# Optimization experiments

Hardware: AMD Instinct MI355X
Metric: run time of the kernel (lower is better)

## Reference

```python
import jax, jax.numpy as jnp
import numpy as np

B, S, DIM = 1, 2048, 2048
NH, NKV, HD = 32, 8, 64
NREP = NH // NKV  # 4


def setup_inputs() -> dict:
    key = jax.random.key(0)
    ks = jax.random.split(key, 5)
    x = jax.random.normal(ks[0], (B, S, DIM), jnp.float32)
    # torch nn.Linear weight layout: (out_features, in_features)
    wq = jax.random.normal(ks[1], (NH * HD, DIM), jnp.float32) * (DIM ** -0.5)
    wk = jax.random.normal(ks[2], (NKV * HD, DIM), jnp.float32) * (DIM ** -0.5)
    wv = jax.random.normal(ks[3], (NKV * HD, DIM), jnp.float32) * (DIM ** -0.5)
    wo = jax.random.normal(ks[4], (DIM, NH * HD), jnp.float32) * ((NH * HD) ** -0.5)
    # Llama-style rotary frequencies: angle[t, i] = t / 10000^(2i/head_dim)
    inv_freq = 1.0 / (10000.0 ** (np.arange(0, HD, 2, dtype=np.float64) / HD))  # (HD/2,)
    ang = np.outer(np.arange(S, dtype=np.float64), inv_freq)                     # (S, HD/2)
    freqs_cis = jnp.asarray(np.stack([np.cos(ang), np.sin(ang)], axis=-1), jnp.float32)  # (S, HD/2, 2)
    # additive causal mask, shape (1, 1, S, S)
    mask = jnp.triu(jnp.full((S, S), -1e9, jnp.float32), k=1)[None, None]
    return dict(x=x, wq=wq, wk=wk, wv=wv, wo=wo, freqs_cis=freqs_cis, mask=mask)


def _apply_rope(x, cos, sin):
    # x: (B, S, H, HD); rotate adjacent pairs along last dim
    xr = x.reshape(x.shape[:-1] + (-1, 2))
    x1, x2 = xr[..., 0], xr[..., 1]
    c = cos[None, :, None, :]  # (1, S, 1, HD/2)
    s = sin[None, :, None, :]
    out = jnp.stack([x1 * c - x2 * s, x1 * s + x2 * c], axis=-1)
    return out.reshape(x.shape)


def reference(x, wq, wk, wv, wo, freqs_cis, mask):
    b, s, _ = x.shape
    q = (x @ wq.T).reshape(b, s, NH, HD)
    k = (x @ wk.T).reshape(b, s, NKV, HD)
    v = (x @ wv.T).reshape(b, s, NKV, HD)
    cos, sin = freqs_cis[..., 0], freqs_cis[..., 1]
    q = _apply_rope(q, cos, sin)
    k = _apply_rope(k, cos, sin)
    # GQA: group q heads by kv head instead of materializing repeated K/V
    qg = q.reshape(b, s, NKV, NREP, HD)
    scale = HD ** -0.5
    # scores: (b, g=kv_head, r=rep, s=q_pos, t=k_pos)
    scores = jnp.einsum('bsgrd,btgd->bgrst', qg, k) * scale
    scores = scores + mask[:, :, None]  # (1,1,1,S,S) broadcast
    p = jax.nn.softmax(scores.astype(jnp.float32), axis=-1).astype(q.dtype)
    out = jnp.einsum('bgrst,btgd->bsgrd', p, v).reshape(b, s, NH * HD)
    return out @ wo.T
```

## Files before the change

### kernel.cpp

```cpp
#include <hip/hip_runtime.h>
#include <hip/hip_bf16.h>

#define S_LEN 2048
#define DIM_  2048
#define NH    32
#define NKV   8
#define HD    64

typedef __bf16 bf16x8 __attribute__((ext_vector_type(8)));
typedef __bf16 bf16x4 __attribute__((ext_vector_type(4)));
typedef float  f32x4  __attribute__((ext_vector_type(4)));

#define AS_GLOBAL(p) ((const __attribute__((address_space(1))) void*)(p))
#define AS_LDS(p)    ((__attribute__((address_space(3))) void*)(p))

__device__ __forceinline__ bf16x8 pack8(float4 a, float4 b) {
  bf16x8 r;
  r[0] = (__bf16)a.x; r[1] = (__bf16)a.y; r[2] = (__bf16)a.z; r[3] = (__bf16)a.w;
  r[4] = (__bf16)b.x; r[5] = (__bf16)b.y; r[6] = (__bf16)b.z; r[7] = (__bf16)b.w;
  return r;
}

__global__ __launch_bounds__(256) void cvt_xw(
    const float* __restrict__ x,  const float* __restrict__ wq,
    const float* __restrict__ wk, const float* __restrict__ wv,
    const float* __restrict__ wo,
    __bf16* __restrict__ xb, __bf16* __restrict__ wb, __bf16* __restrict__ wob)
{
  const size_t stride = 458752;
  size_t base = (size_t)blockIdx.x * 256 + threadIdx.x;
#pragma unroll
  for (int k = 0; k < 4; ++k) {
    size_t i = base + (size_t)k * stride;
    const float* src; __bf16* dst; size_t j;
    if (i < 524288)       { src = x;  dst = xb;            j = i; }
    else if (i < 1048576) { src = wq; dst = wb;            j = i - 524288; }
    else if (i < 1179648) { src = wk; dst = wb + 4194304;  j = i - 1048576; }
    else if (i < 1310720) { src = wv; dst = wb + 5242880;  j = i - 1179648; }
    else                  { src = wo; dst = wob;           j = i - 1310720; }
    float4 f0 = ((const float4*)src)[j * 2];
    float4 f1 = ((const float4*)src)[j * 2 + 1];
    ((bf16x8*)dst)[j ^ ((j >> 8) & 7)] = pack8(f0, f1);
  }
}

#define BK 64
#define TA_ELEMS 8192
#define TB_ELEMS 4096

__device__ __forceinline__ void stage_A(
    const __bf16* __restrict__ g, int row0, int k0, int ld, __bf16* lds)
{
  const int tid = threadIdx.x;
  const int wave = tid >> 6;
#pragma unroll
  for (int iss = 0; iss < 4; ++iss) {
    int off = (iss * 256 + tid) * 16;
    int r = off >> 7;
    int c = (off & 127) >> 1;
    __builtin_amdgcn_global_load_lds(
        AS_GLOBAL(g + (size_t)(row0 + r) * ld + k0 + c),
        AS_LDS(lds + iss * 2048 + wave * 512),
        16, 0, 0);
  }
}

__device__ __forceinline__ void stage_B(
    const __bf16* __restrict__ g, int row0, int k0, int ld, __bf16* lds)
{
  const int tid = threadIdx.x;
  const int wave = tid >> 6;
#pragma unroll
  for (int iss = 0; iss < 2; ++iss) {
    int off = (iss * 256 + tid) * 16;
    int r = off >> 7;
    int c = (off & 127) >> 1;
    __builtin_amdgcn_global_load_lds(
        AS_GLOBAL(g + (size_t)(row0 + r) * ld + k0 + c),
        AS_LDS(lds + iss * 2048 + wave * 512), 16, 0, 0);
  }
}

__device__ __forceinline__ void gemm_mainloop(
    const __bf16* __restrict__ A, const __bf16* __restrict__ B,
    int row0, int col0, int lda, int ldb, int nt,
    __bf16* As, __bf16* Bs, f32x4 acc[4][2])
{
  const int lane = threadIdx.x & 63;
  const int wave = threadIdx.x >> 6;
  const int wr = wave >> 1, wc = wave & 1;
  const int fr = lane & 15, fg = lane >> 4;
  const int sw = fr & 7;

  stage_A(A, row0, 0, lda, As);
  stage_B(B, col0, 0, ldb, Bs);

  for (int t = 0; t < nt; ++t) {
    const int cur = t & 1;
    if (t + 1 < nt) {
      stage_A(A, row0, (t + 1) * BK, lda, As + (cur ^ 1) * TA_ELEMS);
      stage_B(B, col0, (t + 1) * BK, ldb, Bs + (cur ^ 1) * TB_ELEMS);
    }
    __syncthreads();
#pragma unroll
    for (int kk = 0; kk < 2; ++kk) {
      bf16x8 a[4], b[2];
#pragma unroll
      for (int mi = 0; mi < 4; ++mi)
        a[mi] = *(const bf16x8*)(As + cur * TA_ELEMS +
                 (wr * 64 + mi * 16 + fr) * 64 + (((kk * 4 + fg) ^ sw) * 8));
#pragma unroll
      for (int ni = 0; ni < 2; ++ni)
        b[ni] = *(const bf16x8*)(Bs + cur * TB_ELEMS +
                 (wc * 32 + ni * 16 + fr) * 64 + (((kk * 4 + fg) ^ sw) * 8));
#pragma unroll
      for (int mi = 0; mi < 4; ++mi)
#pragma unroll
        for (int ni = 0; ni < 2; ++ni)
          acc[mi][ni] = __builtin_amdgcn_mfma_f32_16x16x32_bf16(a[mi], b[ni], acc[mi][ni], 0, 0, 0);
    }
    __syncthreads();
  }
}

__global__ __launch_bounds__(256) void qkv_gemm(
    const __bf16* __restrict__ xb, const __bf16* __restrict__ wb,
    __bf16* __restrict__ q_buf, __bf16* __restrict__ k_buf, __bf16* __restrict__ v_buf)
{
  __shared__ __bf16 As[2 * TA_ELEMS];
  __shared__ __bf16 Bs[2 * TB_ELEMS];
  const int lane = threadIdx.x & 63;
  const int wave = threadIdx.x >> 6;
  const int wr = wave >> 1, wc = wave & 1;
  const int fr = lane & 15, fg = lane >> 4;

  const int lid = blockIdx.x;
  const int xcd = lid & 7;
  const int i   = lid >> 3;
  const int row0 = (i & 15) * 128;
  const int col0 = (xcd * 6 + (i >> 4)) * 64;

  f32x4 acc[4][2] = {};
  gemm_mainloop(xb, wb, row0, col0, DIM_, DIM_, DIM_ / BK, As, Bs, acc);

  const int rowg0 = row0 + wr * 64;
  const int colg0 = col0 + wc * 32;
#pragma unroll
  for (int mi = 0; mi < 4; ++mi) {
#pragma unroll
    for (int ni = 0; ni < 2; ++ni) {
#pragma unroll
      for (int j = 0; j < 4; ++j) {
        int row = rowg0 + mi * 16 + fg * 4 + j;
        int col = colg0 + ni * 16 + fr;
        float v = acc[mi][ni][j];
        if (col < 2048) {
          int h = col >> 6, d = col & 63;
          q_buf[((size_t)h * S_LEN + row) * HD + d] = (__bf16)v;
        } else if (col < 2560) {
          int c = col - 2048, g = c >> 6, d = c & 63;
          k_buf[((size_t)g * S_LEN + row) * HD + d] = (__bf16)v;
        } else {
          int c = col - 2560, g = c >> 6, d = c & 63;
          v_buf[((size_t)g * HD + d) * S_LEN + row] = (__bf16)v;
        }
      }
    }
  }
}

__global__ __launch_bounds__(256) void oproj_gemm(
    const __bf16* __restrict__ attn_buf, const __bf16* __restrict__ wob,
    float* __restrict__ out)
{
  __shared__ __bf16 As[2 * TA_ELEMS];
  __shared__ __bf16 Bs[2 * TB_ELEMS];
  const int lane = threadIdx.x & 63;
  const int wave = threadIdx.x >> 6;
  const int wr = wave >> 1, wc = wave & 1;
  const int fr = lane & 15, fg = lane >> 4;

  const int lid = blockIdx.x;
  const int xcd = lid & 7;
  const int i   = lid >> 3;
  const int row0 = (i & 15) * 128;
  const int col0 = (xcd * 4 + (i >> 4)) * 64;

  f32x4 acc[4][2] = {};
  gemm_mainloop(attn_buf, wob, row0, col0, DIM_, DIM_, DIM_ / BK, As, Bs, acc);

  const int rowg0 = row0 + wr * 64;
  const int colg0 = col0 + wc * 32;
#pragma unroll
  for (int mi = 0; mi < 4; ++mi)
#pragma unroll
    for (int ni = 0; ni < 2; ++ni)
#pragma unroll
      for (int j = 0; j < 4; ++j) {
        int row = rowg0 + mi * 16 + fg * 4 + j;
        int col = colg0 + ni * 16 + fr;
        out[(size_t)row * DIM_ + col] = acc[mi][ni][j];
      }
}

__global__ __launch_bounds__(256) void rope_k(
    __bf16* __restrict__ k_buf, const float* __restrict__ fc)
{
  int idx = blockIdx.x * 256 + threadIdx.x;
  int i    = idx & 31;
  int sp   = (idx >> 5) & (S_LEN - 1);
  int g    = idx >> 16;
  __bf16* buf = k_buf + ((size_t)g * S_LEN + sp) * HD;
  float c = fc[(sp * 32 + i) * 2 + 0];
  float s = fc[(sp * 32 + i) * 2 + 1];
  float x1 = (float)buf[2 * i], x2 = (float)buf[2 * i + 1];
  buf[2 * i + 0] = (__bf16)(x1 * c - x2 * s);
  buf[2 * i + 1] = (__bf16)(x1 * s + x2 * c);
}

__global__ __launch_bounds__(512) void attn_kernel(
    const __bf16* __restrict__ q_buf, const __bf16* __restrict__ k_buf,
    const __bf16* __restrict__ v_buf, const float* __restrict__ fc,
    __bf16* __restrict__ attn_buf)
{
  __shared__ __align__(16) __bf16 Ks[2][64 * 64];
  __shared__ __align__(16) __bf16 Vs[2][64 * 64];
  __shared__ __align__(16) __bf16 lds_p[8][16][72];

  const int tid  = threadIdx.x;
  const int lane = tid & 63;
  const int wave = tid >> 6;
  const int n = blockIdx.x;
  const int qt = (n < 256) ? (15 - (n >> 5)) : ((n - 256) >> 5);
  const int h  = n & 31;
  const int g = h >> 2;
  const int r0 = qt * 128 + wave * 16;
  const int lrow = lane & 15;
  const int lgrp = lane >> 4;
  const int lk = lgrp * 8;

  const __bf16* qh = q_buf + (size_t)h * S_LEN * HD;
  const __bf16* kh = k_buf + (size_t)g * S_LEN * HD;
  const __bf16* vh = v_buf + (size_t)g * HD * S_LEN;

  const int sr   = tid >> 3;
  const int scol = tid & 7;
  const int dcol = scol ^ (sr & 7);

  const float KS = 0.125f * 1.44269504088896f;
  bf16x8 qa[2];
  const float* fcrow = fc + (size_t)(r0 + lrow) * 64;
#pragma unroll
  for (int kk = 0; kk < 2; ++kk) {
    qa[kk] = *(const bf16x8*)(qh + (size_t)(r0 + lrow) * HD + kk * 32 + lk);
    float4 cs0 = *(const float4*)(fcrow + (kk * 16 + lgrp * 4) * 2);
    float4 cs1 = *(const float4*)(fcrow + (kk * 16 + lgrp * 4) * 2 + 4);
    float cc[4] = {cs0.x * KS, cs0.z * KS, cs1.x * KS, cs1.z * KS};
    float ss[4] = {cs0.y * KS, cs0.w * KS, cs1.y * KS, cs1.w * KS};
#pragma unroll
    for (int pr = 0; pr < 4; ++pr) {
      float x1 = (float)qa[kk][2 * pr], x2 = (float)qa[kk][2 * pr + 1];
      qa[kk][2 * pr]     = (__bf16)(x1 * cc[pr] - x2 * ss[pr]);
      qa[kk][2 * pr + 1] = (__bf16)(x1 * ss[pr] + x2 * cc[pr]);
    }
  }

  float m_col = -3.0e38f, l_col = 0.f;
  f32x4 oacc[4] = {};

  const int nt = 2 * qt + 2;

  {
    uint4 k0 = *(const uint4*)(kh + (size_t)sr * HD + scol * 8);
    uint4 v0 = *(const uint4*)(vh + (size_t)sr * S_LEN + scol * 8);
    *(uint4*)(&Ks[0][sr * 64 + dcol * 8]) = k0;
    *(uint4*)(&Vs[0][sr * 64 + dcol * 8]) = v0;
  }
  __syncthreads();

  for (int t = 0; t < nt; ++t) {
    const int cur = t & 1;
    const int t0 = t * 64;

    const int tn0 = (t + 1 < nt ? t + 1 : t) * 64;
    uint4 kreg = *(const uint4*)(kh + (size_t)(tn0 + sr) * HD + scol * 8);
    uint4 vreg = *(const uint4*)(vh + (size_t)sr * S_LEN + tn0 + scol * 8);

    const int dmax = r0 + 15 - t0;
    if (dmax >= 0) {
      f32x4 sc[4] = {};
      const int cmax = dmax >> 4;
      __builtin_amdgcn_s_setprio(1);
#pragma unroll
      for (int c = 0; c < 4; ++c) {
        if (c <= cmax) {
#pragma unroll
          for (int kk = 0; kk < 2; ++kk) {
            bf16x8 ka = *(const bf16x8*)(
                &Ks[cur][(c * 16 + lrow) * 64 + (((kk * 4 + lgrp) ^ (lrow & 7)) * 8)]);
            sc[c] = __builtin_amdgcn_mfma_f32_16x16x32_bf16(ka, qa[kk], sc[c], 0, 0, 0);
          }
        }
      }
      __builtin_amdgcn_s_setprio(0);

      float p[16];
      const int q = r0 + lrow;
      if (t0 + 63 <= r0) {
#pragma unroll
        for (int c = 0; c < 4; ++c)
#pragma unroll
          for (int j = 0; j < 4; ++j)
            p[c * 4 + j] = sc[c][j];
      } else {
#pragma unroll
        for (int c = 0; c < 4; ++c)
#pragma unroll
          for (int j = 0; j < 4; ++j) {
            int kv = t0 + c * 16 + lgrp * 4 + j;
            p[c * 4 + j] = (kv <= q) ? sc[c][j] : -3.0e38f;
          }
      }

      float m8[8];
#pragma unroll
      for (int i = 0; i < 8; ++i) m8[i] = fmaxf(p[i], p[i + 8]);
      float t1 = fmaxf(fmaxf(m8[0], m8[1]), m8[2]);
      float t2 = fmaxf(fmaxf(m8[3], m8[4]), m8[5]);
      float t3 = fmaxf(m8[6], m8[7]);
      float mx = fmaxf(fmaxf(t1, t2), t3);
      mx = fmaxf(mx, __shfl_xor(mx, 16, 64));
      mx = fmaxf(mx, __shfl_xor(mx, 32, 64));

      if (__all(mx <= m_col + 8.f)) {
      } else {
        float nm = fmaxf(m_col, mx);
        float alpha = __builtin_amdgcn_exp2f(m_col - nm);
        m_col = nm;
        float ar[4];
#pragma unroll
        for (int j = 0; j < 4; ++j)
          ar[j] = __shfl(alpha, lgrp * 4 + j, 64);
#pragma unroll
        for (int nf = 0; nf < 4; ++nf)
#pragma unroll
          for (int j = 0; j < 4; ++j)
            oacc[nf][j] *= ar[j];
        l_col *= alpha;
      }

#pragma unroll
      for (int i = 0; i < 16; ++i)
        p[i] = __builtin_amdgcn_exp2f(p[i] - m_col);
      float s8[8], s4[4];
#pragma unroll
      for (int i = 0; i < 8; ++i) s8[i] = p[i] + p[i + 8];
#pragma unroll
      for (int i = 0; i < 4; ++i) s4[i] = s8[i] + s8[i + 4];
      float rs = (s4[0] + s4[1]) + (s4[2] + s4[3]);
      rs += __shfl_xor(rs, 16, 64);
      rs += __shfl_xor(rs, 32, 64);
      l_col += rs;

#pragma unroll
      for (int c = 0; c < 4; ++c)
#pragma unroll
        for (int e = 0; e < 2; ++e) {
          union { __bf16 hh[2]; unsigned u; } pk;
          pk.hh[0] = (__bf16)p[c * 4 + 2 * e];
          pk.hh[1] = (__bf16)p[c * 4 + 2 * e + 1];
          *(unsigned*)&lds_p[wave][lrow][c * 16 + lgrp * 4 + 2 * e] = pk.u;
        }
      asm volatile("s_waitcnt lgkmcnt(0)" ::: "memory");

      bf16x8 pa0 = *(const bf16x8*)&lds_p[wave][lrow][lk];
      __builtin_amdgcn_s_setprio(1);
#pragma unroll
      for (int nf = 0; nf < 4; ++nf) {
        bf16x8 vb = *(const bf16x8*)(
            &Vs[cur][(nf * 16 + lrow) * 64 + ((lgrp ^ (lrow & 7)) * 8)]);
        oacc[nf] = __builtin_amdgcn_mfma_f32_16x16x32_bf16(pa0, vb, oacc[nf], 0, 0, 0);
      }
      __builtin_amdgcn_s_setprio(0);
      if (dmax >= 32) {
        bf16x8 pa1 = *(const bf16x8*)&lds_p[wave][lrow][32 + lk];
        __builtin_amdgcn_s_setprio(1);
#pragma unroll
        for (int nf = 0; nf < 4; ++nf) {
          bf16x8 vb = *(const bf16x8*)(
              &Vs[cur][(nf * 16 + lrow) * 64 + (((4 + lgrp) ^ (lrow & 7)) * 8)]);
          oacc[nf] = __builtin_amdgcn_mfma_f32_16x16x32_bf16(pa1, vb, oacc[nf], 0, 0, 0);
        }
        __builtin_amdgcn_s_setprio(0);
      }
    }

    *(uint4*)(&Ks[cur ^ 1][sr * 64 + dcol * 8]) = kreg;
    *(uint4*)(&Vs[cur ^ 1][sr * 64 + dcol * 8]) = vreg;
    __syncthreads();
  }

  float rlr[4];
#pragma unroll
  for (int j = 0; j < 4; ++j)
    rlr[j] = 1.0f / __shfl(l_col, lgrp * 4 + j, 64);
#pragma unroll
  for (int nf = 0; nf < 4; ++nf)
#pragma unroll
    for (int j = 0; j < 4; ++j) {
      int row = r0 + lgrp * 4 + j;
      int col = h * HD + nf * 16 + lrow;
      int ch  = (((col >> 3) & 7) ^ (row & 7));
      int cols = (col & 7) | (ch << 3) | (col & ~63);
      attn_buf[(size_t)row * (NH * HD) + cols] =
          (__bf16)(oacc[nf][j] * rlr[j]);
    }
}

extern "C" void kernel_launch(void* const* d_in, const int* in_sizes, int n_in,
                              void* d_out, int out_size, void* d_ws, size_t ws_size,
                              hipStream_t stream)
{
  const float* x  = (const float*)d_in[0];
  const float* wq = (const float*)d_in[1];
  const float* wk = (const float*)d_in[2];
  const float* wv = (const float*)d_in[3];
  const float* wo = (const float*)d_in[4];
  const float* fc = (const float*)d_in[5];
  float* out = (float*)d_out;

  char* ws = (char*)d_ws;
  __bf16* q_buf    = (__bf16*)(ws);
  __bf16* k_buf    = (__bf16*)(ws +  8u * 1024 * 1024);
  __bf16* v_buf    = (__bf16*)(ws + 10u * 1024 * 1024);
  __bf16* attn_buf = (__bf16*)(ws + 12u * 1024 * 1024);
  __bf16* xb       = (__bf16*)(ws + 20u * 1024 * 1024);
  __bf16* wb       = (__bf16*)(ws + 28u * 1024 * 1024);
  __bf16* wob      = (__bf16*)(ws + 40u * 1024 * 1024);

  cvt_xw<<<dim3(1792), 256, 0, stream>>>(x, wq, wk, wv, wo, xb, wb, wob);
  qkv_gemm<<<dim3(768), 256, 0, stream>>>(xb, wb, q_buf, k_buf, v_buf);
  rope_k<<<dim3(2048), 256, 0, stream>>>(k_buf, fc);
  attn_kernel<<<dim3(512), 512, 0, stream>>>(q_buf, k_buf, v_buf, fc, attn_buf);
  oproj_gemm<<<dim3(512), 256, 0, stream>>>(attn_buf, wob, out);
}
```

Before: 136.8 us.

## Shrink attention blocks to 64-query tiles with 4 waves, doubling grid

The attention kernel moves from 512-thread blocks covering 128 query rows to 256-thread blocks covering 64 query rows, launching 1024 blocks instead of 512. Each thread now stages two K/V chunks per tile, and the per-wave skip of fully masked tiles is dropped because every wave in a 64-row block needs all of its tiles up to the diagonal. Blocks are ordered longest-first, replacing the earlier paired ordering. The aim is better load balance across the causal triangle and more resident blocks per CU, at the cost of loading each K/V tile once per 64 query rows rather than once per 128.

Measured after the change: 147.1 us. 1.08x slower.

```diff
diff --git a/kernel.cpp b/kernel.cpp
--- a/kernel.cpp
+++ b/kernel.cpp
@@ -60,8 +60,7 @@
     int c = (off & 127) >> 1;
     __builtin_amdgcn_global_load_lds(
         AS_GLOBAL(g + (size_t)(row0 + r) * ld + k0 + c),
-        AS_LDS(lds + iss * 2048 + wave * 512),
-        16, 0, 0);
+        AS_LDS(lds + iss * 2048 + wave * 512), 16, 0, 0);
   }
 }
 
@@ -218,23 +217,23 @@
   buf[2 * i + 1] = (__bf16)(x1 * s + x2 * c);
 }
 
-__global__ __launch_bounds__(512) void attn_kernel(
+__global__ __launch_bounds__(256) void attn_kernel(
     const __bf16* __restrict__ q_buf, const __bf16* __restrict__ k_buf,
     const __bf16* __restrict__ v_buf, const float* __restrict__ fc,
     __bf16* __restrict__ attn_buf)
 {
   __shared__ __align__(16) __bf16 Ks[2][64 * 64];
   __shared__ __align__(16) __bf16 Vs[2][64 * 64];
-  __shared__ __align__(16) __bf16 lds_p[8][16][72];
+  __shared__ __align__(16) __bf16 lds_p[4][16][72];
 
   const int tid  = threadIdx.x;
   const int lane = tid & 63;
   const int wave = tid >> 6;
   const int n = blockIdx.x;
-  const int qt = (n < 256) ? (15 - (n >> 5)) : ((n - 256) >> 5);
+  const int qt = 31 - (n >> 5);
   const int h  = n & 31;
   const int g = h >> 2;
-  const int r0 = qt * 128 + wave * 16;
+  const int r0 = qt * 64 + wave * 16;
   const int lrow = lane & 15;
   const int lgrp = lane >> 4;
   const int lk = lgrp * 8;
@@ -243,9 +242,6 @@
   const __bf16* kh = k_buf + (size_t)g * S_LEN * HD;
   const __bf16* vh = v_buf + (size_t)g * HD * S_LEN;
 
-  const int sr   = tid >> 3;
-  const int scol = tid & 7;
-  const int dcol = scol ^ (sr & 7);
 
   const float KS = 0.125f * 1.44269504088896f;
   bf16x8 qa[2];
@@ -268,9 +264,12 @@
   float m_col = -3.0e38f, l_col = 0.f;
   f32x4 oacc[4] = {};
 
-  const int nt = 2 * qt + 2;
-
-  {
+  const int nt = qt + 1;
+
+#pragma unroll
+  for (int iss = 0; iss < 2; ++iss) {
+    int ci = iss * 256 + tid;
+    int sr = ci >> 3, scol = ci & 7, dcol = scol ^ (sr & 7);
     uint4 k0 = *(const uint4*)(kh + (size_t)sr * HD + scol * 8);
     uint4 v0 = *(const uint4*)(vh + (size_t)sr * S_LEN + scol * 8);
     *(uint4*)(&Ks[0][sr * 64 + dcol * 8]) = k0;
@@ -283,120 +282,129 @@
     const int t0 = t * 64;
 
     const int tn0 = (t + 1 < nt ? t + 1 : t) * 64;
-    uint4 kreg = *(const uint4*)(kh + (size_t)(tn0 + sr) * HD + scol * 8);
-    uint4 vreg = *(const uint4*)(vh + (size_t)sr * S_LEN + tn0 + scol * 8);
+    uint4 kreg[2], vreg[2];
+#pragma unroll
+    for (int iss = 0; iss < 2; ++iss) {
+      int ci = iss * 256 + tid;
+      int sr = ci >> 3, scol = ci & 7;
+      kreg[iss] = *(const uint4*)(kh + (size_t)(tn0 + sr) * HD + scol * 8);
+      vreg[iss] = *(const uint4*)(vh + (size_t)sr * S_LEN + tn0 + scol * 8);
+    }
 
     const int dmax = r0 + 15 - t0;
-    if (dmax >= 0) {
-      f32x4 sc[4] = {};
-      const int cmax = dmax >> 4;
-      __builtin_amdgcn_s_setprio(1);
-#pragma unroll
-      for (int c = 0; c < 4; ++c) {
-        if (c <= cmax) {
-#pragma unroll
-          for (int kk = 0; kk < 2; ++kk) {
-            bf16x8 ka = *(const bf16x8*)(
-                &Ks[cur][(c * 16 + lrow) * 64 + (((kk * 4 + lgrp) ^ (lrow & 7)) * 8)]);
-            sc[c] = __builtin_amdgcn_mfma_f32_16x16x32_bf16(ka, qa[kk], sc[c], 0, 0, 0);
-          }
+    const int cmax = dmax >> 4;
+    f32x4 sc[4] = {};
+    __builtin_amdgcn_s_setprio(1);
+#pragma unroll
+    for (int c = 0; c < 4; ++c) {
+      if (c <= cmax) {
+#pragma unroll
+        for (int kk = 0; kk < 2; ++kk) {
+          bf16x8 ka = *(const bf16x8*)(
+              &Ks[cur][(c * 16 + lrow) * 64 + (((kk * 4 + lgrp) ^ (lrow & 7)) * 8)]);
+          sc[c] = __builtin_amdgcn_mfma_f32_16x16x32_bf16(ka, qa[kk], sc[c], 0, 0, 0);
         }
       }
-      __builtin_amdgcn_s_setprio(0);
-
-      float p[16];
-      const int q = r0 + lrow;
-      if (t0 + 63 <= r0) {
-#pragma unroll
-        for (int c = 0; c < 4; ++c)
-#pragma unroll
-          for (int j = 0; j < 4; ++j)
-            p[c * 4 + j] = sc[c][j];
-      } else {
-#pragma unroll
-        for (int c = 0; c < 4; ++c)
-#pragma unroll
-          for (int j = 0; j < 4; ++j) {
-            int kv = t0 + c * 16 + lgrp * 4 + j;
-            p[c * 4 + j] = (kv <= q) ? sc[c][j] : -3.0e38f;
-          }
+    }
+    __builtin_amdgcn_s_setprio(0);
+
+    float p[16];
+    const int q = r0 + lrow;
+    if (t0 + 63 <= r0) {
+#pragma unroll
+      for (int c = 0; c < 4; ++c)
+#pragma unroll
+        for (int j = 0; j < 4; ++j)
+          p[c * 4 + j] = sc[c][j];
+    } else {
+#pragma unroll
+      for (int c = 0; c < 4; ++c)
+#pragma unroll
+        for (int j = 0; j < 4; ++j) {
+          int kv = t0 + c * 16 + lgrp * 4 + j;
+          p[c * 4 + j] = (kv <= q) ? sc[c][j] : -3.0e38f;
+        }
+    }
+
+    float m8[8];
+#pragma unroll
+    for (int i = 0; i < 8; ++i) m8[i] = fmaxf(p[i], p[i + 8]);
+    float t1 = fmaxf(fmaxf(m8[0], m8[1]), m8[2]);
+    float t2 = fmaxf(fmaxf(m8[3], m8[4]), m8[5]);
+    float t3 = fmaxf(m8[6], m8[7]);
+    float mx = fmaxf(fmaxf(t1, t2), t3);
+    mx = fmaxf(mx, __shfl_xor(mx, 16, 64));
+    mx = fmaxf(mx, __shfl_xor(mx, 32, 64));
+
+    if (__all(mx <= m_col + 8.f)) {
+    } else {
+      float nm = fmaxf(m_col, mx);
+      float alpha = __builtin_amdgcn_exp2f(m_col - nm);
+      m_col = nm;
+      float ar[4];
+#pragma unroll
+      for (int j = 0; j < 4; ++j)
+        ar[j] = __shfl(alpha, lgrp * 4 + j, 64);
+#pragma unroll
+      for (int nf = 0; nf < 4; ++nf)
+#pragma unroll
+        for (int j = 0; j < 4; ++j)
+          oacc[nf][j] *= ar[j];
+      l_col *= alpha;
+    }
+
+#pragma unroll
+    for (int i = 0; i < 16; ++i)
+      p[i] = __builtin_amdgcn_exp2f(p[i] - m_col);
+    float s8[8], s4[4];
+#pragma unroll
+    for (int i = 0; i < 8; ++i) s8[i] = p[i] + p[i + 8];
+#pragma unroll
+    for (int i = 0; i < 4; ++i) s4[i] = s8[i] + s8[i + 4];
+    float rs = (s4[0] + s4[1]) + (s4[2] + s4[3]);
+    rs += __shfl_xor(rs, 16, 64);
+    rs += __shfl_xor(rs, 32, 64);
+    l_col += rs;
+
+#pragma unroll
+    for (int c = 0; c < 4; ++c)
+#pragma unroll
+      for (int e = 0; e < 2; ++e) {
+        union { __bf16 hh[2]; unsigned u; } pk;
+        pk.hh[0] = (__bf16)p[c * 4 + 2 * e];
+        pk.hh[1] = (__bf16)p[c * 4 + 2 * e + 1];
+        *(unsigned*)&lds_p[wave][lrow][c * 16 + lgrp * 4 + 2 * e] = pk.u;
       }
-
-      float m8[8];
-#pragma unroll
-      for (int i = 0; i < 8; ++i) m8[i] = fmaxf(p[i], p[i + 8]);
-      float t1 = fmaxf(fmaxf(m8[0], m8[1]), m8[2]);
-      float t2 = fmaxf(fmaxf(m8[3], m8[4]), m8[5]);
-      float t3 = fmaxf(m8[6], m8[7]);
-      float mx = fmaxf(fmaxf(t1, t2), t3);
-      mx = fmaxf(mx, __shfl_xor(mx, 16, 64));
-      mx = fmaxf(mx, __shfl_xor(mx, 32, 64));
-
-      if (__all(mx <= m_col + 8.f)) {
-      } else {
-        float nm = fmaxf(m_col, mx);
-        float alpha = __builtin_amdgcn_exp2f(m_col - nm);
-        m_col = nm;
-        float ar[4];
-#pragma unroll
-        for (int j = 0; j < 4; ++j)
-          ar[j] = __shfl(alpha, lgrp * 4 + j, 64);
-#pragma unroll
-        for (int nf = 0; nf < 4; ++nf)
-#pragma unroll
-          for (int j = 0; j < 4; ++j)
-            oacc[nf][j] *= ar[j];
-        l_col *= alpha;
-      }
-
-#pragma unroll
-      for (int i = 0; i < 16; ++i)
-        p[i] = __builtin_amdgcn_exp2f(p[i] - m_col);
-      float s8[8], s4[4];
-#pragma unroll
-      for (int i = 0; i < 8; ++i) s8[i] = p[i] + p[i + 8];
-#pragma unroll
-      for (int i = 0; i < 4; ++i) s4[i] = s8[i] + s8[i + 4];
-      float rs = (s4[0] + s4[1]) + (s4[2] + s4[3]);
-      rs += __shfl_xor(rs, 16, 64);
-      rs += __shfl_xor(rs, 32, 64);
-      l_col += rs;
-
-#pragma unroll
-      for (int c = 0; c < 4; ++c)
-#pragma unroll
-        for (int e = 0; e < 2; ++e) {
-          union { __bf16 hh[2]; unsigned u; } pk;
-          pk.hh[0] = (__bf16)p[c * 4 + 2 * e];
-          pk.hh[1] = (__bf16)p[c * 4 + 2 * e + 1];
-          *(unsigned*)&lds_p[wave][lrow][c * 16 + lgrp * 4 + 2 * e] = pk.u;
-        }
-      asm volatile("s_waitcnt lgkmcnt(0)" ::: "memory");
-
-      bf16x8 pa0 = *(const bf16x8*)&lds_p[wave][lrow][lk];
+    asm volatile("s_waitcnt lgkmcnt(0)" ::: "memory");
+
+    bf16x8 pa0 = *(const bf16x8*)&lds_p[wave][lrow][lk];
+    __builtin_amdgcn_s_setprio(1);
+#pragma unroll
+    for (int nf = 0; nf < 4; ++nf) {
+      bf16x8 vb = *(const bf16x8*)(
+          &Vs[cur][(nf * 16 + lrow) * 64 + ((lgrp ^ (lrow & 7)) * 8)]);
+      oacc[nf] = __builtin_amdgcn_mfma_f32_16x16x32_bf16(pa0, vb, oacc[nf], 0, 0, 0);
+    }
+    __builtin_amdgcn_s_setprio(0);
+    if (dmax >= 32) {
+      bf16x8 pa1 = *(const bf16x8*)&lds_p[wave][lrow][32 + lk];
       __builtin_amdgcn_s_setprio(1);
 #pragma unroll
       for (int nf = 0; nf < 4; ++nf) {
         bf16x8 vb = *(const bf16x8*)(
-            &Vs[cur][(nf * 16 + lrow) * 64 + ((lgrp ^ (lrow & 7)) * 8)]);
-        oacc[nf] = __builtin_amdgcn_mfma_f32_16x16x32_bf16(pa0, vb, oacc[nf], 0, 0, 0);
+            &Vs[cur][(nf * 16 + lrow) * 64 + (((4 + lgrp) ^ (lrow & 7)) * 8)]);
+        oacc[nf] = __builtin_amdgcn_mfma_f32_16x16x32_bf16(pa1, vb, oacc[nf], 0, 0, 0);
       }
       __builtin_amdgcn_s_setprio(0);
-      if (dmax >= 32) {
-        bf16x8 pa1 = *(const bf16x8*)&lds_p[wave][lrow][32 + lk];
-        __builtin_amdgcn_s_setprio(1);
-#pragma unroll
-        for (int nf = 0; nf < 4; ++nf) {
-          bf16x8 vb = *(const bf16x8*)(
-              &Vs[cur][(nf * 16 + lrow) * 64 + (((4 + lgrp) ^ (lrow & 7)) * 8)]);
-          oacc[nf] = __builtin_amdgcn_mfma_f32_16x16x32_bf16(pa1, vb, oacc[nf], 0, 0, 0);
-        }
-        __builtin_amdgcn_s_setprio(0);
-      }
-    }
-
-    *(uint4*)(&Ks[cur ^ 1][sr * 64 + dcol * 8]) = kreg;
-    *(uint4*)(&Vs[cur ^ 1][sr * 64 + dcol * 8]) = vreg;
+    }
+
+#pragma unroll
+    for (int iss = 0; iss < 2; ++iss) {
+      int ci = iss * 256 + tid;
+      int sr = ci >> 3, scol = ci & 7, dcol = scol ^ (sr & 7);
+      *(uint4*)(&Ks[cur ^ 1][sr * 64 + dcol * 8]) = kreg[iss];
+      *(uint4*)(&Vs[cur ^ 1][sr * 64 + dcol * 8]) = vreg[iss];
+    }
     __syncthreads();
   }
 
@@ -441,6 +449,6 @@
   cvt_xw<<<dim3(1792), 256, 0, stream>>>(x, wq, wk, wv, wo, xb, wb, wob);
   qkv_gemm<<<dim3(768), 256, 0, stream>>>(xb, wb, q_buf, k_buf, v_buf);
   rope_k<<<dim3(2048), 256, 0, stream>>>(k_buf, fc);
-  attn_kernel<<<dim3(512), 512, 0, stream>>>(q_buf, k_buf, v_buf, fc, attn_buf);
+  attn_kernel<<<dim3(1024), 256, 0, stream>>>(q_buf, k_buf, v_buf, fc, attn_buf);
   oproj_gemm<<<dim3(512), 256, 0, stream>>>(attn_buf, wob, out);
 }
```
